# Optimization experiments

Hardware: AMD Instinct MI355X
Metric: run time of the kernel (lower is better)

The kernel has to match this reference:

```python
import jax, jax.numpy as jnp
import numpy as np

NUM_NODES = 64
NUM_VISIBLE = 16
NUM_STEPS = 20
ENERGY_SCALE = 1.0


def setup_inputs() -> dict:
    key = jax.random.key(0)
    k1, k2, k3, k4 = jax.random.split(key, 4)
    B, E = 65536, 512
    embedding = jax.random.normal(k1, (B, E), dtype=jnp.float32)
    reward = jax.random.normal(k2, (B,), dtype=jnp.float32)
    pca_components = jax.random.normal(k3, (E, NUM_VISIBLE), dtype=jnp.float32)
    quadratic = jax.random.normal(k4, (NUM_NODES, NUM_NODES), dtype=jnp.float32) * 0.01
    return {"embedding": embedding, "reward": reward,
            "pca_components": pca_components, "quadratic": quadratic}


def reference(embedding, reward, pca_components, quadratic):
    B = embedding.shape[0]
    dtype = embedding.dtype

    # KPP fallback transform: PCA-style projection (B, E) @ (E, 16) -> (B, 16)
    rep = embedding @ pca_components
    visible_bias = rep[:, :NUM_VISIBLE]

    # per-sample linear bias, zeros except visible slots; BM bias = batch mean (no_grad)
    lb = jnp.zeros((B, NUM_NODES), dtype).at[:, :NUM_VISIBLE].set(visible_bias)
    b = jax.lax.stop_gradient(lb.mean(axis=0))  # (N,)

    # clamped visible state: sigmoid(2*r) broadcast to (B, NUM_VISIBLE)
    s_visible = jnp.broadcast_to(jax.nn.sigmoid(reward[:, None] * 2.0), (B, NUM_VISIBLE))

    Wsym = quadratic + quadratic.T  # symmetric coupling field

    key = jax.random.key(42)
    k_init, k_scan = jax.random.split(key)
    hidden0 = jax.random.bernoulli(k_init, 0.5, (B, NUM_NODES - NUM_VISIBLE)).astype(dtype)
    s0 = jnp.concatenate([s_visible, hidden0], axis=-1)  # (B, N)

    def gibbs_step(s, k):
        p = jax.nn.sigmoid(s @ Wsym + b)               # (B, N)
        s_new = jax.random.bernoulli(k, p).astype(dtype)
        s_new = s_new.at[:, :NUM_VISIBLE].set(s_visible)  # clamp visible units
        return s_new, None

    keys = jax.random.split(k_scan, NUM_STEPS)
    s_all, _ = jax.lax.scan(gibbs_step, s0, keys)

    # energy E(s) = -s^T Q s - b^T s  per sample
    energy = -jnp.einsum('bi,ij,bj->b', s_all, quadratic, s_all) - s_all @ b

    adjusted = reward - ENERGY_SCALE * energy
    return adjusted[:, None]  # (B, 1)
```

## Files before the change

### kernel.cpp

```cpp
#include <hip/hip_runtime.h>
#include <stdint.h>

#define NNODES 64
#define NVIS   16
#define NHID   48
#define NSTEPS 20
#define BATCH  65536
#define EDIM   512

typedef float f32x2 __attribute__((ext_vector_type(2)));
typedef float f32x4 __attribute__((ext_vector_type(4)));

__device__ __forceinline__ f32x2 pk_fma_lo(f32x2 s, f32x2 w, f32x2 c) {
  f32x2 d;
  asm("v_pk_fma_f32 %0, %1, %2, %3 op_sel:[0,0,0] op_sel_hi:[1,0,1]"
      : "=v"(d) : "v"(s), "v"(w), "v"(c));
  return d;
}
__device__ __forceinline__ f32x2 pk_fma_hi(f32x2 s, f32x2 w, f32x2 c) {
  f32x2 d;
  asm("v_pk_fma_f32 %0, %1, %2, %3 op_sel:[0,1,0] op_sel_hi:[1,1,1]"
      : "=v"(d) : "v"(s), "v"(w), "v"(c));
  return d;
}
__device__ __forceinline__ f32x2 pk_fma2(f32x2 a, f32x2 b, f32x2 c) {
  f32x2 d;
  asm("v_pk_fma_f32 %0, %1, %2, %3" : "=v"(d) : "v"(a), "v"(b), "v"(c));
  return d;
}
__device__ __forceinline__ f32x2 pk_mul2(f32x2 a, f32x2 b) {
  f32x2 d;
  asm("v_pk_mul_f32 %0, %1, %2" : "=v"(d) : "v"(a), "v"(b));
  return d;
}
__device__ __forceinline__ f32x2 pk_add2(f32x2 a, f32x2 b) {
  f32x2 d;
  asm("v_pk_add_f32 %0, %1, %2" : "=v"(d) : "v"(a), "v"(b));
  return d;
}
__device__ __forceinline__ f32x2 pk_sub2(f32x2 a, f32x2 b) {
  f32x2 d;
  asm("v_pk_add_f32 %0, %1, %2 neg_lo:[0,1] neg_hi:[0,1]" : "=v"(d) : "v"(a), "v"(b));
  return d;
}
__device__ __forceinline__ f32x2 pk_negsub2(f32x2 a, f32x2 b) {
  f32x2 d;
  asm("v_pk_add_f32 %0, %1, %2 neg_lo:[1,1] neg_hi:[1,1]" : "=v"(d) : "v"(a), "v"(b));
  return d;
}

__device__ __forceinline__ void tf2x32(uint32_t k0, uint32_t k1,
                                       uint32_t x0, uint32_t x1,
                                       uint32_t& o0, uint32_t& o1) {
  const uint32_t ks0 = k0, ks1 = k1, ks2 = k0 ^ k1 ^ 0x1BD11BDAu;
  x0 += ks0; x1 += ks1;
  const int rotA[4] = {13, 15, 26, 6};
  const int rotB[4] = {17, 29, 16, 24};
#pragma unroll
  for (int i = 0; i < 5; ++i) {
#pragma unroll
    for (int r = 0; r < 4; ++r) {
      const int rot = (i & 1) ? rotB[r] : rotA[r];
      x0 += x1;
      x1 = __builtin_rotateleft32(x1, rot);
      x1 ^= x0;
    }
    const uint32_t i0 = (i == 0 || i == 3) ? ks1 : (i == 1 || i == 4) ? ks2 : ks0;
    const uint32_t i1 = (i == 0 || i == 3) ? ks2 : (i == 1 || i == 4) ? ks0 : ks1;
    x0 += i0;
    x1 += i1 + (uint32_t)(i + 1);
  }
  o0 = x0; o1 = x1;
}

__device__ __forceinline__ uint32_t rbits32(uint32_t k0, uint32_t k1, uint32_t n) {
  uint32_t a, b;
  tf2x32(k0, k1, 0u, n, a, b);
  return a ^ b;
}

__device__ __forceinline__ f32x2 sigmoid2_pk(f32x2 a) {
#pragma clang fp contract(off)
  const f32x2 cL2En  = (f32x2)(-1.44269504088896341f);
  const f32x2 cHalf  = (f32x2)0.5f;
  const f32x2 cLn2Hi = (f32x2)0.693359375f;
  const f32x2 cLn2Lo = (f32x2)(-2.12194440e-4f);
  const f32x2 c0 = (f32x2)1.9875691500e-4f, c1 = (f32x2)1.3981999507e-3f;
  const f32x2 c2 = (f32x2)8.3334519073e-3f, c3 = (f32x2)4.1665795894e-2f;
  const f32x2 c4 = (f32x2)1.6666665459e-1f, c5 = (f32x2)5.0000001201e-1f;
  const f32x2 cOne = (f32x2)1.0f;

  f32x2 t = pk_fma2(a, cL2En, cHalf);
  f32x2 fx; fx.x = floorf(t.x); fx.y = floorf(t.y);
  f32x2 tmp = pk_mul2(fx, cLn2Hi);
  f32x2 z   = pk_mul2(fx, cLn2Lo);
  f32x2 xr  = pk_negsub2(a, tmp);
  xr = pk_sub2(xr, z);
  f32x2 zz = pk_mul2(xr, xr);
  f32x2 y = pk_fma2(xr, c0, c1);
  y = pk_fma2(y, xr, c2);
  y = pk_fma2(y, xr, c3);
  y = pk_fma2(y, xr, c4);
  y = pk_fma2(y, xr, c5);
  y = pk_fma2(y, zz, xr);
  y = pk_add2(y, cOne);
  int mx = (int)fx.x, my = (int)fx.y;
  f32x2 e;
  e.x = __int_as_float((mx + 127) << 23);
  e.y = __int_as_float((my + 127) << 23);
  f32x2 ex = pk_mul2(y, e);
  f32x2 den = pk_add2(ex, cOne);
  f32x2 r;
  r.x = 1.0f / den.x;
  r.y = 1.0f / den.y;
  return r;
}

__device__ __forceinline__ void dot4(const f32x4* st,
                                     const f32x2* wp, f32x2 a16A, f32x2 a16B,
                                     f32x2& oA, f32x2& oB) {
  f32x2 accA = a16A, accB = a16B;
#pragma unroll
  for (int i = 0; i < 24; ++i) {
    f32x4 q0 = st[2 * i];
    f32x4 q1 = st[2 * i + 1];
    f32x2 q0A; q0A.x = q0.x; q0A.y = q0.y;
    f32x2 q0B; q0B.x = q0.z; q0B.y = q0.w;
    f32x2 q1A; q1A.x = q1.x; q1A.y = q1.y;
    f32x2 q1B; q1B.x = q1.z; q1B.y = q1.w;
    accA = pk_fma_lo(q0A, wp[i], accA);
    accA = pk_fma_hi(q1A, wp[i], accA);
    accB = pk_fma_lo(q0B, wp[i], accB);
    accB = pk_fma_hi(q1B, wp[i], accB);
  }
  oA = accA; oB = accB;
}

__global__ __launch_bounds__(512) void colsum_kernel(const float4* __restrict__ emb4,
                                                     float4* __restrict__ partials4,
                                                     int nblk) {
  __shared__ float4 red[4][128];
  const int t = threadIdx.x;
  const int c4 = t & 127, rs = t >> 7;
  float4 acc = make_float4(0.f, 0.f, 0.f, 0.f);
  const int stride = nblk * 4;
  for (int r = blockIdx.x * 4 + rs; r < BATCH; r += stride) {
    float4 v = emb4[(size_t)r * 128 + c4];
    acc.x += v.x; acc.y += v.y; acc.z += v.z; acc.w += v.w;
  }
  red[rs][c4] = acc;
  __syncthreads();
  if (rs == 0) {
    float4 a = red[0][c4], b = red[1][c4], c = red[2][c4], d = red[3][c4];
    float4 s;
    s.x = (a.x + b.x) + (c.x + d.x);
    s.y = (a.y + b.y) + (c.y + d.y);
    s.z = (a.z + b.z) + (c.z + d.z);
    s.w = (a.w + b.w) + (c.w + d.w);
    partials4[(size_t)blockIdx.x * 128 + c4] = s;
  }
}

__global__ __launch_bounds__(512) void reduce_kernel(const float* __restrict__ partials,
                                                     float* __restrict__ level2, int per) {
  const int t = threadIdx.x;
  float a = 0.0f;
  const int s0 = blockIdx.x * per;
  for (int s = s0; s < s0 + per; ++s) a += partials[(size_t)s * EDIM + t];
  level2[(size_t)blockIdx.x * EDIM + t] = a;
}

__global__ __launch_bounds__(512) void prep_kernel(const float* __restrict__ pca,
                                                   const float* __restrict__ level2, int g2,
                                                   float* __restrict__ bvec,
                                                   unsigned* __restrict__ keys) {
  __shared__ float cs[EDIM];
  int t = threadIdx.x;
  float a = 0.0f;
  for (int i = 0; i < g2; ++i) a += level2[(size_t)i * EDIM + t];
  cs[t] = a;
  __syncthreads();
  if (t < NNODES) {
    float bj = 0.0f;
    if (t < NVIS) {
      for (int e = 0; e < EDIM; ++e) bj = fmaf(cs[e], pca[e * NVIS + t], bj);
      bj *= (1.0f / 65536.0f);
    }
    bvec[t] = bj;
  }
  if (t == 0) {
    uint32_t ki0, ki1, ks0, ks1;
    tf2x32(0u, 42u, 0u, 0u, ki0, ki1);
    tf2x32(0u, 42u, 0u, 1u, ks0, ks1);
    keys[0] = ki0; keys[1] = ki1;
    for (int s = 0; s < NSTEPS; ++s) {
      uint32_t y0, y1;
      tf2x32(ks0, ks1, 0u, (uint32_t)s, y0, y1);
      keys[2 + 2 * s] = y0;
      keys[3 + 2 * s] = y1;
    }
  }
}

__global__ __launch_bounds__(256) void gibbs_kernel(const float* __restrict__ reward,
                                                    const float* __restrict__ quadratic,
                                                    const float* __restrict__ bvec,
                                                    const unsigned* __restrict__ keys,
                                                    float* __restrict__ out) {
#pragma clang fp contract(off)
  __shared__ float Wl[NNODES][NNODES];
  __shared__ alignas(16) f32x4 sbuf[4][NHID];

  const int tid = threadIdx.x;
  for (int i = tid; i < NNODES * NNODES; i += 256) {
    int k = i >> 6, j = i & 63;
    Wl[k][j] = quadratic[i] + quadratic[j * NNODES + k];
  }
  __syncthreads();

  const int wave = tid >> 6, lane = tid & 63;
  const int gw = blockIdx.x * 4 + wave;
  const int r0 = gw * 4;

  const float4 rw4 = ((const float4*)reward)[gw];
  const float bj = bvec[lane];
  f32x2 svA = sigmoid2_pk((f32x2){rw4.x * 2.0f, rw4.y * 2.0f});
  f32x2 svB = sigmoid2_pk((f32x2){rw4.z * 2.0f, rw4.w * 2.0f});

  f32x2 wp[24];
#pragma unroll
  for (int i = 0; i < 24; ++i) {
    f32x2 w; w.x = Wl[16 + 2 * i][lane]; w.y = Wl[17 + 2 * i][lane];
    wp[i] = w;
  }
  f32x2 acc16A = (f32x2)0.0f, acc16B = (f32x2)0.0f;
#pragma unroll
  for (int i = 0; i < 8; ++i) {
    f32x2 w; w.x = Wl[2 * i][lane]; w.y = Wl[2 * i + 1][lane];
    acc16A = pk_fma_lo(svA, w, acc16A);
    acc16A = pk_fma_hi(svA, w, acc16A);
    acc16B = pk_fma_lo(svB, w, acc16B);
    acc16B = pk_fma_hi(svB, w, acc16B);
  }

  f32x4* sbw = sbuf[wave];
  const f32x4* st = sbw;

  uint32_t nn[3];
  uint32_t ni[3];
  float*   uw[3];
#pragma unroll
  for (int c = 0; c < 3; ++c) {
    int idx = c * 64 + lane;
    int rr = (idx * 683) >> 15;
    int jj = idx - rr * 48;
    nn[c] = (uint32_t)((r0 + rr) * NNODES + NVIS + jj);
    ni[c] = (uint32_t)((r0 + rr) * NHID + jj);
    uw[c] = ((float*)sbw) + (jj * 4 + rr);
  }

  const bool isvis = (lane < NVIS);
  const int jc = isvis ? 0 : lane - NVIS;
  f32x2 scurA = svA, scurB = svB;

  {
    const uint32_t ki0 = keys[0], ki1 = keys[1];
#pragma unroll
    for (int c = 0; c < 3; ++c) {
      uint32_t b = rbits32(ki0, ki1, ni[c]);
      *uw[c] = (b >> 31) ? 0.0f : 1.0f;
    }
  }

  const uint2* kbuf = (const uint2*)(keys + 2);
  uint2 kk = kbuf[0];
#pragma unroll 1
  for (int t = 0; t < NSTEPS; ++t) {
    uint2 kn = kbuf[(t + 1 < NSTEPS) ? t + 1 : t];

    f32x2 aA, aB;
    dot4(st, wp, acc16A, acc16B, aA, aB);

    uint32_t b0 = rbits32(kk.x, kk.y, nn[0]);
    uint32_t b1 = rbits32(kk.x, kk.y, nn[1]);
    uint32_t b2 = rbits32(kk.x, kk.y, nn[2]);
    *uw[0] = __uint_as_float((b0 >> 9) | 0x3f800000u) - 1.0f;
    *uw[1] = __uint_as_float((b1 >> 9) | 0x3f800000u) - 1.0f;
    *uw[2] = __uint_as_float((b2 >> 9) | 0x3f800000u) - 1.0f;

    f32x2 pA = sigmoid2_pk(aA);
    f32x2 pB = sigmoid2_pk(aB);

    f32x4 uq = sbw[jc];
    if (!isvis) {
      scurA.x = (uq.x < pA.x) ? 1.0f : 0.0f;
      scurA.y = (uq.y < pA.y) ? 1.0f : 0.0f;
      scurB.x = (uq.z < pB.x) ? 1.0f : 0.0f;
      scurB.y = (uq.w < pB.y) ? 1.0f : 0.0f;
      f32x4 sq; sq.x = scurA.x; sq.y = scurA.y; sq.z = scurB.x; sq.w = scurB.y;
      sbw[jc] = sq;
    }
    kk = kn;
  }

  f32x2 aA, aB;
  dot4(st, wp, acc16A, acc16B, aA, aB);
  f32x2 bj2; bj2.x = bj; bj2.y = bj;
  const f32x2 half2 = (f32x2)0.5f;
  f32x2 cA = pk_mul2(scurA, pk_fma2(half2, aA, bj2));
  f32x2 cB = pk_mul2(scurB, pk_fma2(half2, aB, bj2));
  float c0 = cA.x, c1 = cA.y, c2 = cB.x, c3 = cB.y;
#pragma unroll
  for (int off = 32; off; off >>= 1) {
    c0 += __shfl_xor(c0, off);
    c1 += __shfl_xor(c1, off);
    c2 += __shfl_xor(c2, off);
    c3 += __shfl_xor(c3, off);
  }
  if (lane == 0) {
    ((float4*)out)[gw] = make_float4(rw4.x + c0, rw4.y + c1, rw4.z + c2, rw4.w + c3);
  }
}

extern "C" void kernel_launch(void* const* d_in, const int* in_sizes, int n_in,
                              void* d_out, int out_size, void* d_ws, size_t ws_size,
                              hipStream_t stream) {
  const float* emb    = (const float*)d_in[0];
  const float* reward = (const float*)d_in[1];
  const float* pca    = (const float*)d_in[2];
  const float* quad   = (const float*)d_in[3];
  float* out = (float*)d_out;

  int nblk = 1024;
  while (nblk > 4 &&
         ws_size < (size_t)nblk * EDIM * 4 + (size_t)64 * EDIM * 4 + 4096)
    nblk >>= 1;
  const int g2  = (nblk >= 64) ? 64 : nblk;
  const int per = nblk / g2;

  float*    partials = (float*)d_ws;
  float*    level2   = partials + (size_t)nblk * EDIM;
  float*    bvec     = level2 + (size_t)64 * EDIM;
  unsigned* keys     = (unsigned*)(bvec + NNODES);

  colsum_kernel<<<nblk, 512, 0, stream>>>((const float4*)emb, (float4*)partials, nblk);
  reduce_kernel<<<g2, 512, 0, stream>>>(partials, level2, per);
  prep_kernel<<<1, 512, 0, stream>>>(pca, level2, g2, bvec, keys);
  gibbs_kernel<<<BATCH / 16, 256, 0, stream>>>(reward, quad, bvec, keys, out);
}
```

Before: 321.4 us.

## Store hidden Gibbs state as packed bytes and split uniform buffer

Hidden state per wave is now kept in LDS as one byte per sample, four samples packed in a uint32 per hidden node, instead of four floats. The dot product reads 12 uint4 words instead of 48 float4 and unpacks them with v_cvt_f32_ubyteN. Uniforms move to a separate float buffer, the RNG writes now come before the dot product, and the launch bound requests 4 blocks per CU. This cuts LDS read traffic per step but adds conversion ALU instructions and a possible race in the reordering.

Measured after the change: 398.7 us. 1.24x slower.

```diff
diff --git a/kernel.cpp b/kernel.cpp
--- a/kernel.cpp
+++ b/kernel.cpp
@@ -47,6 +47,19 @@
   f32x2 d;
   asm("v_pk_add_f32 %0, %1, %2 neg_lo:[1,1] neg_hi:[1,1]" : "=v"(d) : "v"(a), "v"(b));
   return d;
+}
+
+__device__ __forceinline__ float cvt_ub0(uint32_t d) {
+  float f; asm("v_cvt_f32_ubyte0 %0, %1" : "=v"(f) : "v"(d)); return f;
+}
+__device__ __forceinline__ float cvt_ub1(uint32_t d) {
+  float f; asm("v_cvt_f32_ubyte1 %0, %1" : "=v"(f) : "v"(d)); return f;
+}
+__device__ __forceinline__ float cvt_ub2(uint32_t d) {
+  float f; asm("v_cvt_f32_ubyte2 %0, %1" : "=v"(f) : "v"(d)); return f;
+}
+__device__ __forceinline__ float cvt_ub3(uint32_t d) {
+  float f; asm("v_cvt_f32_ubyte3 %0, %1" : "=v"(f) : "v"(d)); return f;
 }
 
 __device__ __forceinline__ void tf2x32(uint32_t k0, uint32_t k1,
@@ -116,22 +129,37 @@
   return r;
 }
 
-__device__ __forceinline__ void dot4(const f32x4* st,
-                                     const f32x2* wp, f32x2 a16A, f32x2 a16B,
-                                     f32x2& oA, f32x2& oB) {
+__device__ __forceinline__ void dot_bytes(const uint4* st,
+                                          const f32x2* wp, f32x2 a16A, f32x2 a16B,
+                                          f32x2& oA, f32x2& oB) {
   f32x2 accA = a16A, accB = a16B;
 #pragma unroll
-  for (int i = 0; i < 24; ++i) {
-    f32x4 q0 = st[2 * i];
-    f32x4 q1 = st[2 * i + 1];
-    f32x2 q0A; q0A.x = q0.x; q0A.y = q0.y;
-    f32x2 q0B; q0B.x = q0.z; q0B.y = q0.w;
-    f32x2 q1A; q1A.x = q1.x; q1A.y = q1.y;
-    f32x2 q1B; q1B.x = q1.z; q1B.y = q1.w;
-    accA = pk_fma_lo(q0A, wp[i], accA);
-    accA = pk_fma_hi(q1A, wp[i], accA);
-    accB = pk_fma_lo(q0B, wp[i], accB);
-    accB = pk_fma_hi(q1B, wp[i], accB);
+  for (int i = 0; i < 12; ++i) {
+    uint4 q = st[i];
+    {
+      f32x2 sA; sA.x = cvt_ub0(q.x); sA.y = cvt_ub1(q.x);
+      f32x2 sB; sB.x = cvt_ub2(q.x); sB.y = cvt_ub3(q.x);
+      accA = pk_fma_lo(sA, wp[2 * i], accA);
+      accB = pk_fma_lo(sB, wp[2 * i], accB);
+    }
+    {
+      f32x2 sA; sA.x = cvt_ub0(q.y); sA.y = cvt_ub1(q.y);
+      f32x2 sB; sB.x = cvt_ub2(q.y); sB.y = cvt_ub3(q.y);
+      accA = pk_fma_hi(sA, wp[2 * i], accA);
+      accB = pk_fma_hi(sB, wp[2 * i], accB);
+    }
+    {
+      f32x2 sA; sA.x = cvt_ub0(q.z); sA.y = cvt_ub1(q.z);
+      f32x2 sB; sB.x = cvt_ub2(q.z); sB.y = cvt_ub3(q.z);
+      accA = pk_fma_lo(sA, wp[2 * i + 1], accA);
+      accB = pk_fma_lo(sB, wp[2 * i + 1], accB);
+    }
+    {
+      f32x2 sA; sA.x = cvt_ub0(q.w); sA.y = cvt_ub1(q.w);
+      f32x2 sB; sB.x = cvt_ub2(q.w); sB.y = cvt_ub3(q.w);
+      accA = pk_fma_hi(sA, wp[2 * i + 1], accA);
+      accB = pk_fma_hi(sB, wp[2 * i + 1], accB);
+    }
   }
   oA = accA; oB = accB;
 }
@@ -202,14 +230,15 @@
   }
 }
 
-__global__ __launch_bounds__(256) void gibbs_kernel(const float* __restrict__ reward,
-                                                    const float* __restrict__ quadratic,
-                                                    const float* __restrict__ bvec,
-                                                    const unsigned* __restrict__ keys,
-                                                    float* __restrict__ out) {
+__global__ __launch_bounds__(256, 4) void gibbs_kernel(const float* __restrict__ reward,
+                                                       const float* __restrict__ quadratic,
+                                                       const float* __restrict__ bvec,
+                                                       const unsigned* __restrict__ keys,
+                                                       float* __restrict__ out) {
 #pragma clang fp contract(off)
   __shared__ float Wl[NNODES][NNODES];
-  __shared__ alignas(16) f32x4 sbuf[4][NHID];
+  __shared__ float ubuf[4][4 * NHID];
+  __shared__ alignas(16) uint32_t sbyte[4][NHID];
 
   const int tid = threadIdx.x;
   for (int i = tid; i < NNODES * NNODES; i += 256) {
@@ -243,12 +272,14 @@
     acc16B = pk_fma_hi(svB, w, acc16B);
   }
 
-  f32x4* sbw = sbuf[wave];
-  const f32x4* st = sbw;
+  float* ubw = ubuf[wave];
+  uint32_t* sw32 = sbyte[wave];
+  const uint4* stq = (const uint4*)sw32;
 
   uint32_t nn[3];
   uint32_t ni[3];
   float*   uw[3];
+  int      sb_off[3];
 #pragma unroll
   for (int c = 0; c < 3; ++c) {
     int idx = c * 64 + lane;
@@ -256,31 +287,29 @@
     int jj = idx - rr * 48;
     nn[c] = (uint32_t)((r0 + rr) * NNODES + NVIS + jj);
     ni[c] = (uint32_t)((r0 + rr) * NHID + jj);
-    uw[c] = ((float*)sbw) + (jj * 4 + rr);
+    uw[c] = ubw + idx;
+    sb_off[c] = jj * 4 + rr;
   }
 
   const bool isvis = (lane < NVIS);
   const int jc = isvis ? 0 : lane - NVIS;
-  f32x2 scurA = svA, scurB = svB;
 
   {
     const uint32_t ki0 = keys[0], ki1 = keys[1];
+    volatile uint8_t* sb8 = (volatile uint8_t*)sw32;
 #pragma unroll
     for (int c = 0; c < 3; ++c) {
       uint32_t b = rbits32(ki0, ki1, ni[c]);
-      *uw[c] = (b >> 31) ? 0.0f : 1.0f;
-    }
-  }
-
+      sb8[sb_off[c]] = (uint8_t)((b >> 31) ^ 1u);
+    }
+  }
+
+  uint32_t dcur = 0;
   const uint2* kbuf = (const uint2*)(keys + 2);
   uint2 kk = kbuf[0];
 #pragma unroll 1
   for (int t = 0; t < NSTEPS; ++t) {
     uint2 kn = kbuf[(t + 1 < NSTEPS) ? t + 1 : t];
-
-    f32x2 aA, aB;
-    dot4(st, wp, acc16A, acc16B, aA, aB);
-
     uint32_t b0 = rbits32(kk.x, kk.y, nn[0]);
     uint32_t b1 = rbits32(kk.x, kk.y, nn[1]);
     uint32_t b2 = rbits32(kk.x, kk.y, nn[2]);
@@ -288,23 +317,31 @@
     *uw[1] = __uint_as_float((b1 >> 9) | 0x3f800000u) - 1.0f;
     *uw[2] = __uint_as_float((b2 >> 9) | 0x3f800000u) - 1.0f;
 
+    f32x2 aA, aB;
+    dot_bytes(stq, wp, acc16A, acc16B, aA, aB);
     f32x2 pA = sigmoid2_pk(aA);
     f32x2 pB = sigmoid2_pk(aB);
 
-    f32x4 uq = sbw[jc];
+    f32x2 uA; uA.x = ubw[jc];            uA.y = ubw[NHID + jc];
+    f32x2 uB; uB.x = ubw[2 * NHID + jc]; uB.y = ubw[3 * NHID + jc];
     if (!isvis) {
-      scurA.x = (uq.x < pA.x) ? 1.0f : 0.0f;
-      scurA.y = (uq.y < pA.y) ? 1.0f : 0.0f;
-      scurB.x = (uq.z < pB.x) ? 1.0f : 0.0f;
-      scurB.y = (uq.w < pB.y) ? 1.0f : 0.0f;
-      f32x4 sq; sq.x = scurA.x; sq.y = scurA.y; sq.z = scurB.x; sq.w = scurB.y;
-      sbw[jc] = sq;
+      uint32_t e0 = (uA.x < pA.x) ? 1u : 0u;
+      uint32_t e1 = (uA.y < pA.y) ? 1u : 0u;
+      uint32_t e2 = (uB.x < pB.x) ? 1u : 0u;
+      uint32_t e3 = (uB.y < pB.y) ? 1u : 0u;
+      dcur = e0 | (e1 << 8) | (e2 << 16) | (e3 << 24);
+      sw32[jc] = dcur;
     }
     kk = kn;
   }
 
   f32x2 aA, aB;
-  dot4(st, wp, acc16A, acc16B, aA, aB);
+  dot_bytes(stq, wp, acc16A, acc16B, aA, aB);
+  f32x2 scurA = svA, scurB = svB;
+  if (!isvis) {
+    scurA.x = cvt_ub0(dcur); scurA.y = cvt_ub1(dcur);
+    scurB.x = cvt_ub2(dcur); scurB.y = cvt_ub3(dcur);
+  }
   f32x2 bj2; bj2.x = bj; bj2.y = bj;
   const f32x2 half2 = (f32x2)0.5f;
   f32x2 cA = pk_mul2(scurA, pk_fma2(half2, aA, bj2));
```
